# Performance work log

Measured on AMD Instinct MI355X. Metric: run time of the kernel, lower is better.

The kernel has to match this reference:

```python
import jax, jax.numpy as jnp
import numpy as np

TEMPERATURE = 0.05
BETA = 1.0
LAMBDA_THRESHOLD = 0.7
EPS = 1e-8


def setup_inputs() -> dict:
    key = jax.random.key(0)
    k1, k2 = jax.random.split(key)
    B, D = 8192, 256
    features = jax.random.normal(k1, (B, D), dtype=jnp.float32)
    labels = jax.random.randint(k2, (B,), 0, 100, dtype=jnp.int64)
    return {"features": features, "labels": labels}


def reference(features, labels):
    B = features.shape[0]
    # L2-normalize rows
    f = features / jnp.linalg.norm(features, axis=1, keepdims=True)
    sim = jnp.matmul(f, f.T) / TEMPERATURE                      # [B, B]
    pos_mask = (labels[:, None] == labels[None, :]).astype(f.dtype)
    eye = jnp.eye(B, dtype=f.dtype)
    pos_mask = pos_mask - eye                                    # positives, no diagonal
    exp_sim = jnp.exp(sim) * (1.0 - eye)                         # diag zeroed
    denom = jnp.sum(exp_sim, axis=1, keepdims=True)              # [B, 1]
    # SCL term: -sum over positive pairs of log(exp_sim[i,j] / (denom_i + eps))
    # log(exp_sim/(denom+eps)) = sim - log(denom+eps) for off-diagonal entries
    per_pair = jnp.log(denom + EPS) - sim                        # [B, B]
    num_pos = jnp.sum(pos_mask)
    scl_loss = jnp.sum(pos_mask * per_pair)
    scl_loss = jnp.where(num_pos > 0, scl_loss / num_pos, 0.0)
    # Relaxation term: rows with too-similar positives
    high_sim = ((sim * TEMPERATURE) > LAMBDA_THRESHOLD) & (pos_mask > 0)
    high_f = high_sim.astype(f.dtype)
    row_sum = jnp.sum(exp_sim * high_f, axis=1)                  # [B]
    self_term = jnp.exp(jnp.asarray(1.0 / TEMPERATURE, dtype=f.dtype))
    row_log = jnp.where(row_sum > 0, jnp.log(row_sum + self_term), 0.0)
    n_high = jnp.sum(high_f)
    relax_loss = jnp.where(n_high > 0, jnp.sum(row_log) / n_high, 0.0)
    total = scl_loss + BETA * relax_loss
    return total
```

## Files before the change

### kernel.cpp

```cpp
#include <hip/hip_runtime.h>
#include <hip/hip_bf16.h>
#include <math.h>

typedef short bf16x8 __attribute__((ext_vector_type(8)));
typedef float f32x16 __attribute__((ext_vector_type(16)));

#define NB 8192
#define ND 256
#define NCLSR 100
#define BK 64
#define ES 136
#define INV_T 20.0f
#define LOG2E_T 28.853900817779268f
#define HI_THR 1.2026042e6f
#define SELF_TERM 4.85165195e8f


__global__ __launch_bounds__(256) void normalize_kernel(
    const float* __restrict__ feat, unsigned short* __restrict__ fb,
    float* __restrict__ hsum, float* __restrict__ nhighf,
    float* __restrict__ scal) {
    const int wave = threadIdx.x >> 6;
    const int lane = threadIdx.x & 63;
    const int row  = blockIdx.x * 4 + wave;
    float4 v = reinterpret_cast<const float4*>(feat + (size_t)row * ND)[lane];
    float ss = v.x * v.x + v.y * v.y + v.z * v.z + v.w * v.w;
    #pragma unroll
    for (int off = 32; off > 0; off >>= 1) ss += __shfl_xor(ss, off);
    const float inv = rsqrtf(ss);
    ushort4 o;
    __hip_bfloat16 h0 = __float2bfloat16(v.x * inv); o.x = *reinterpret_cast<unsigned short*>(&h0);
    __hip_bfloat16 h1 = __float2bfloat16(v.y * inv); o.y = *reinterpret_cast<unsigned short*>(&h1);
    __hip_bfloat16 h2 = __float2bfloat16(v.z * inv); o.z = *reinterpret_cast<unsigned short*>(&h2);
    __hip_bfloat16 h3 = __float2bfloat16(v.w * inv); o.w = *reinterpret_cast<unsigned short*>(&h3);
    reinterpret_cast<ushort4*>(fb + (size_t)row * ND)[lane] = o;
    if (blockIdx.x < 32) {
        const int i = (blockIdx.x << 8) + threadIdx.x;
        hsum[i] = 0.f;
        nhighf[i] = 0.f;
    } else if (blockIdx.x == 32 && threadIdx.x < 6) {
        scal[threadIdx.x] = 0.f;
    }
}

__global__ __launch_bounds__(512, 2) void sim_kernel(
    const unsigned short* __restrict__ fb, const int* __restrict__ labels,
    float* __restrict__ Q, float* __restrict__ hsum,
    float* __restrict__ nhighf, float* __restrict__ scal) {
    __shared__ __align__(16) unsigned short ldsU[128 * ES];
    __shared__ float ldsCol[2][128];
    __shared__ float ldsRowF[128];
    __shared__ int   ldsLab[256];
    __shared__ float ldsP[8];
    unsigned short* ldsA = ldsU;
    unsigned short* ldsB = ldsU + 128 * BK;
    unsigned short* ldsE = ldsU;

    const int t = blockIdx.x;
    int bi = (int)((sqrtf((float)(8 * t + 1)) - 1.0f) * 0.5f);
    while ((bi + 1) * (bi + 2) / 2 <= t) ++bi;
    while (bi * (bi + 1) / 2 > t) --bi;
    const int bj = t - bi * (bi + 1) / 2;
    const int I0 = bi << 7;
    const int J0 = bj << 7;
    const bool isdiag = (bi == bj);

    const int tid  = threadIdx.x;
    const int wave = tid >> 6;
    const int lane = tid & 63;
    const int wy = wave >> 2;
    const int wx = wave & 3;
    const int l31  = lane & 31;
    const int half = lane >> 5;

    if (tid < 128) ldsLab[tid] = labels[I0 + tid];
    else if (tid < 256) ldsLab[tid] = labels[J0 + tid - 128];

    int offRC[2];
    #pragma unroll
    for (int c = 0; c < 2; ++c) {
        const int Lg = (c << 6) + lane;
        const int row_loc = (wave << 4) + (Lg >> 3);
        const int g = (Lg & 7) ^ ((Lg >> 3) & 7);
        offRC[c] = row_loc * ND + (g << 3);
    }
    const unsigned short* baseA = fb + (size_t)I0 * ND;
    const unsigned short* baseB = fb + (size_t)J0 * ND;

    f32x16 acc[2];
    #pragma unroll
    for (int fy = 0; fy < 2; ++fy)
        #pragma unroll
        for (int e = 0; e < 16; ++e) acc[fy][e] = 0.f;

    for (int kk = 0; kk < ND; kk += BK) {
        __syncthreads();
        #pragma unroll
        for (int c = 0; c < 2; ++c) {
            __builtin_amdgcn_global_load_lds(
                (const __attribute__((address_space(1))) void*)(baseA + offRC[c] + kk),
                (__attribute__((address_space(3))) void*)(ldsA + (wave << 10) + (c << 9)),
                16, 0, 0);
            __builtin_amdgcn_global_load_lds(
                (const __attribute__((address_space(1))) void*)(baseB + offRC[c] + kk),
                (__attribute__((address_space(3))) void*)(ldsB + (wave << 10) + (c << 9)),
                16, 0, 0);
        }
        __syncthreads();

        #pragma unroll
        for (int s = 0; s < 4; ++s) {
            const int gp = ((s << 1) + half) ^ (l31 & 7);
            const int rowB = (wx << 5) + l31;
            bf16x8 b = *reinterpret_cast<const bf16x8*>(ldsB + rowB * BK + (gp << 3));
            bf16x8 a[2];
            #pragma unroll
            for (int fy = 0; fy < 2; ++fy) {
                const int rowA = (wy << 6) + (fy << 5) + l31;
                a[fy] = *reinterpret_cast<const bf16x8*>(ldsA + rowA * BK + (gp << 3));
            }
            #pragma unroll
            for (int fy = 0; fy < 2; ++fy)
                acc[fy] = __builtin_amdgcn_mfma_f32_32x32x16_bf16(a[fy], b, acc[fy], 0, 0, 0);
        }
    }
    __syncthreads();

    const int ccol = (wx << 5) + l31;
    const int lcol = ldsLab[128 + ccol];
    unsigned short* ePtr = ldsE + (half << 2) * ES + ccol;

    float cs = 0.f;
    float pp = 0.f;

    if (!isdiag) {
        #pragma unroll
        for (int fy = 0; fy < 2; ++fy) {
            const int rbase = (wy << 6) + (fy << 5) + (half << 2);
            int4 lr[4];
            #pragma unroll
            for (int g = 0; g < 4; ++g)
                lr[g] = *reinterpret_cast<const int4*>(&ldsLab[rbase + (g << 3)]);
            #pragma unroll
            for (int reg = 0; reg < 16; ++reg) {
                const int g = reg >> 2, idx = reg & 3;
                const int lrow = (idx == 0) ? lr[g].x : (idx == 1) ? lr[g].y
                               : (idx == 2) ? lr[g].z : lr[g].w;
                const float a = acc[fy][reg];
                const float e = exp2f(a * LOG2E_T);
                cs += e;
                if (lcol == lrow) pp += a;
                __hip_bfloat16 h = __float2bfloat16(e);
                const int roff = (wy << 6) + (fy << 5) + idx + (g << 3);
                ePtr[roff * ES] = *reinterpret_cast<unsigned short*>(&h);
            }
        }
    } else {
        #pragma unroll
        for (int fy = 0; fy < 2; ++fy) {
            const bool dband = (((wy << 1) + fy) == wx);
            #pragma unroll
            for (int reg = 0; reg < 16; ++reg) {
                const int rloc = (reg & 3) + ((reg >> 2) << 3) + (half << 2);
                const int row_local = (wy << 6) + (fy << 5) + rloc;
                const int lrow = ldsLab[row_local];
                const float a = acc[fy][reg];
                const bool diag_el = dband && (l31 == rloc);
                float e = exp2f(a * LOG2E_T);
                if (diag_el) e = 0.f;
                cs += e;
                if (lcol == lrow && !diag_el) pp += a;
                __hip_bfloat16 h = __float2bfloat16(e);
                ldsE[row_local * ES + ccol] = *reinterpret_cast<unsigned short*>(&h);
            }
        }
    }
    const int anyhigh = (cs > HI_THR);
    cs += __shfl_xor(cs, 32);
    if (half == 0) ldsCol[wy][ccol] = cs;
    #pragma unroll
    for (int off = 32; off > 0; off >>= 1) pp += __shfl_xor(pp, off);
    if (lane == 0) ldsP[wave] = pp;

    __syncthreads();

    if (wave < 4) {
        bf16x8 ones;
        #pragma unroll
        for (int j = 0; j < 8; ++j) ones[j] = (short)0x3F80;
        f32x16 rs;
        #pragma unroll
        for (int e = 0; e < 16; ++e) rs[e] = 0.f;
        const int rE = (wave << 5) + l31;
        const unsigned short* rPtr = ldsE + rE * ES + (half << 3);
        #pragma unroll
        for (int kc = 0; kc < 8; ++kc) {
            bf16x8 bE = *reinterpret_cast<const bf16x8*>(rPtr + (kc << 4));
            rs = __builtin_amdgcn_mfma_f32_32x32x16_bf16(ones, bE, rs, 0, 0, 0);
        }
        if (half == 0) ldsRowF[rE] = rs[0];
    }
    __syncthreads();

    if (tid < 128) {
        Q[(size_t)(bi * 64 + bj) * 128 + tid] = ldsRowF[tid];
    } else if (tid < 256 && !isdiag) {
        const int c2 = tid - 128;
        Q[(size_t)(bj * 64 + bi) * 128 + c2] = ldsCol[0][c2] + ldsCol[1][c2];
    }
    if (tid == 0) {
        const float scale = isdiag ? 1.f : 2.f;
        atomicAdd(&scal[0], (ldsP[0] + ldsP[1] + ldsP[2] + ldsP[3] +
                             ldsP[4] + ldsP[5] + ldsP[6] + ldsP[7]) * scale);
    }

    if (__any(anyhigh)) {
        #pragma unroll
        for (int fy = 0; fy < 2; ++fy) {
            const bool dband = isdiag && (((wy << 1) + fy) == wx);
            #pragma unroll
            for (int reg = 0; reg < 16; ++reg) {
                const int rloc = (reg & 3) + ((reg >> 2) << 3) + (half << 2);
                const int row_local = (wy << 6) + (fy << 5) + rloc;
                const int lrow = ldsLab[row_local];
                const float a = acc[fy][reg];
                const bool diag_el = dband && (l31 == rloc);
                if (a > 0.7f && lcol == lrow && !diag_el) {
                    const float e2 = exp2f(a * LOG2E_T);
                    atomicAdd(&hsum[I0 + row_local], e2);
                    atomicAdd(&nhighf[I0 + row_local], 1.f);
                    if (!isdiag) {
                        atomicAdd(&hsum[J0 + ccol], e2);
                        atomicAdd(&nhighf[J0 + ccol], 1.f);
                    }
                }
            }
        }
    }
}

__global__ __launch_bounds__(256) void finalize_kernel(
    const float* __restrict__ Q, const float* __restrict__ hsum,
    const float* __restrict__ nhighf, const int* __restrict__ labels,
    float* __restrict__ scal, float* __restrict__ out) {
    const int g = blockIdx.x;
    const int tid = threadIdx.x;
    __shared__ int cnt[128];
    if (tid < 128) cnt[tid] = 0;
    __syncthreads();
    for (int i = tid; i < NB; i += 256)
        atomicAdd(&cnt[labels[i]], 1);
    const int r = tid & 127;
    const int sh = tid >> 7;
    const float* base = Q + (size_t)g * 64 * 128;
    float s = 0.f;
    #pragma unroll 8
    for (int i = 0; i < 32; ++i)
        s += base[(size_t)(sh * 32 + i) * 128 + r];
    __shared__ float red[256];
    red[tid] = s;
    __syncthreads();
    float SL = 0.f, RL = 0.f, NH = 0.f, NT = 0.f;
    if (tid < 128) {
        const float denom = red[tid] + red[tid + 128];
        const int i = (g << 7) + tid;
        const float np = (float)(cnt[labels[i]] - 1);
        SL = np * logf(denom + 1e-8f);
        const float h = hsum[i];
        if (h > 0.f) RL = logf(h + SELF_TERM);
        NH = nhighf[i];
    }
    if (g == 0 && tid < NCLSR) {
        const float nc = (float)cnt[tid];
        NT = nc * (nc - 1.f);
    }
    #pragma unroll
    for (int off = 32; off > 0; off >>= 1) {
        SL += __shfl_xor(SL, off); RL += __shfl_xor(RL, off);
        NH += __shfl_xor(NH, off); NT += __shfl_xor(NT, off);
    }
    __shared__ float part[4][4];
    if ((tid & 63) == 0) {
        int w = tid >> 6;
        part[w][0] = SL; part[w][1] = RL; part[w][2] = NH; part[w][3] = NT;
    }
    __syncthreads();
    if (tid == 0) {
        float sl = part[0][0] + part[1][0] + part[2][0] + part[3][0];
        float rl = part[0][1] + part[1][1] + part[2][1] + part[3][1];
        float nh = part[0][2] + part[1][2] + part[2][2] + part[3][2];
        float nt = part[0][3] + part[1][3] + part[2][3] + part[3][3];
        atomicAdd(&scal[1], sl);
        atomicAdd(&scal[2], rl);
        atomicAdd(&scal[3], nh);
        if (g == 0) atomicAdd(&scal[4], nt);
        __threadfence();
        const int ticket = atomicAdd((int*)(scal + 5), 1);
        if (ticket == 63) {
            const float SLt = atomicAdd(&scal[1], 0.f);
            const float RLt = atomicAdd(&scal[2], 0.f);
            const float NHt = atomicAdd(&scal[3], 0.f);
            const float NTt = atomicAdd(&scal[4], 0.f);
            const float pos = atomicAdd(&scal[0], 0.f) * INV_T;
            const float scl   = (NTt > 0.f) ? (SLt - pos) / NTt : 0.f;
            const float relax = (NHt > 0.f) ? RLt / NHt : 0.f;
            out[0] = scl + relax;
        }
    }
}

extern "C" void kernel_launch(void* const* d_in, const int* in_sizes, int n_in,
                              void* d_out, int out_size, void* d_ws, size_t ws_size,
                              hipStream_t stream) {
    const float* feat  = (const float*)d_in[0];
    const int* labels  = (const int*)d_in[1];
    float* out = (float*)d_out;

    char* ws = (char*)d_ws;
    unsigned short* fb = (unsigned short*)ws;
    float* Q      = (float*)(ws + (size_t)NB * ND * sizeof(unsigned short));
    float* hsum   = Q + 64 * 64 * 128;
    float* nhighf = hsum + NB;
    float* scal   = nhighf + NB;

    normalize_kernel<<<NB / 4, 256, 0, stream>>>(feat, fb, hsum, nhighf, scal);
    sim_kernel<<<2080, 512, 0, stream>>>(fb, labels, Q, hsum, nhighf, scal);
    finalize_kernel<<<64, 256, 0, stream>>>(Q, hsum, nhighf, labels, scal, out);
}
```

Baseline: 119.0 us.

## Fuse normalize, similarity and finalize into one cooperative persistent kernel

Merges the three kernels into one cooperatively launched persistent kernel. Grid-wide syncs separate the normalization phase, the tile loop and the final reduction. Blocks loop over the 2080 triangular tiles with a grid sized from occupancy (blocks per CU times 256), and the finalize phase runs on the first 64 blocks with 512 threads. This removes two kernel launches and their gaps, at the cost of grid-sync overhead, a persistent tile loop that may balance work less evenly, and cooperative-launch occupancy limits.

```diff
diff --git a/kernel.cpp b/kernel.cpp
--- a/kernel.cpp
+++ b/kernel.cpp
@@ -1,6 +1,9 @@
 #include <hip/hip_runtime.h>
 #include <hip/hip_bf16.h>
+#include <hip/hip_cooperative_groups.h>
 #include <math.h>
+
+namespace cg = cooperative_groups;
 
 typedef short bf16x8 __attribute__((ext_vector_type(8)));
 typedef float f32x16 __attribute__((ext_vector_type(16)));
@@ -10,43 +13,18 @@
 #define NCLSR 100
 #define BK 64
 #define ES 136
+#define NTILE 2080
 #define INV_T 20.0f
 #define LOG2E_T 28.853900817779268f
 #define HI_THR 1.2026042e6f
 #define SELF_TERM 4.85165195e8f
 
 
-__global__ __launch_bounds__(256) void normalize_kernel(
-    const float* __restrict__ feat, unsigned short* __restrict__ fb,
+__global__ __launch_bounds__(512, 2) void fused_kernel(
+    const float* __restrict__ feat, const int* __restrict__ labels,
+    unsigned short* __restrict__ fb, float* __restrict__ Q,
     float* __restrict__ hsum, float* __restrict__ nhighf,
-    float* __restrict__ scal) {
-    const int wave = threadIdx.x >> 6;
-    const int lane = threadIdx.x & 63;
-    const int row  = blockIdx.x * 4 + wave;
-    float4 v = reinterpret_cast<const float4*>(feat + (size_t)row * ND)[lane];
-    float ss = v.x * v.x + v.y * v.y + v.z * v.z + v.w * v.w;
-    #pragma unroll
-    for (int off = 32; off > 0; off >>= 1) ss += __shfl_xor(ss, off);
-    const float inv = rsqrtf(ss);
-    ushort4 o;
-    __hip_bfloat16 h0 = __float2bfloat16(v.x * inv); o.x = *reinterpret_cast<unsigned short*>(&h0);
-    __hip_bfloat16 h1 = __float2bfloat16(v.y * inv); o.y = *reinterpret_cast<unsigned short*>(&h1);
-    __hip_bfloat16 h2 = __float2bfloat16(v.z * inv); o.z = *reinterpret_cast<unsigned short*>(&h2);
-    __hip_bfloat16 h3 = __float2bfloat16(v.w * inv); o.w = *reinterpret_cast<unsigned short*>(&h3);
-    reinterpret_cast<ushort4*>(fb + (size_t)row * ND)[lane] = o;
-    if (blockIdx.x < 32) {
-        const int i = (blockIdx.x << 8) + threadIdx.x;
-        hsum[i] = 0.f;
-        nhighf[i] = 0.f;
-    } else if (blockIdx.x == 32 && threadIdx.x < 6) {
-        scal[threadIdx.x] = 0.f;
-    }
-}
-
-__global__ __launch_bounds__(512, 2) void sim_kernel(
-    const unsigned short* __restrict__ fb, const int* __restrict__ labels,
-    float* __restrict__ Q, float* __restrict__ hsum,
-    float* __restrict__ nhighf, float* __restrict__ scal) {
+    float* __restrict__ scal, float* __restrict__ out) {
     __shared__ __align__(16) unsigned short ldsU[128 * ES];
     __shared__ float ldsCol[2][128];
     __shared__ float ldsRowF[128];
@@ -56,15 +34,6 @@
     unsigned short* ldsB = ldsU + 128 * BK;
     unsigned short* ldsE = ldsU;
 
-    const int t = blockIdx.x;
-    int bi = (int)((sqrtf((float)(8 * t + 1)) - 1.0f) * 0.5f);
-    while ((bi + 1) * (bi + 2) / 2 <= t) ++bi;
-    while (bi * (bi + 1) / 2 > t) --bi;
-    const int bj = t - bi * (bi + 1) / 2;
-    const int I0 = bi << 7;
-    const int J0 = bj << 7;
-    const bool isdiag = (bi == bj);
-
     const int tid  = threadIdx.x;
     const int wave = tid >> 6;
     const int lane = tid & 63;
@@ -73,8 +42,26 @@
     const int l31  = lane & 31;
     const int half = lane >> 5;
 
-    if (tid < 128) ldsLab[tid] = labels[I0 + tid];
-    else if (tid < 256) ldsLab[tid] = labels[J0 + tid - 128];
+    for (int row = blockIdx.x * 8 + wave; row < NB; row += gridDim.x * 8) {
+        float4 v = reinterpret_cast<const float4*>(feat + (size_t)row * ND)[lane];
+        float ss = v.x * v.x + v.y * v.y + v.z * v.z + v.w * v.w;
+        #pragma unroll
+        for (int off = 32; off > 0; off >>= 1) ss += __shfl_xor(ss, off);
+        const float inv = rsqrtf(ss);
+        ushort4 o;
+        __hip_bfloat16 h0 = __float2bfloat16(v.x * inv); o.x = *reinterpret_cast<unsigned short*>(&h0);
+        __hip_bfloat16 h1 = __float2bfloat16(v.y * inv); o.y = *reinterpret_cast<unsigned short*>(&h1);
+        __hip_bfloat16 h2 = __float2bfloat16(v.z * inv); o.z = *reinterpret_cast<unsigned short*>(&h2);
+        __hip_bfloat16 h3 = __float2bfloat16(v.w * inv); o.w = *reinterpret_cast<unsigned short*>(&h3);
+        reinterpret_cast<ushort4*>(fb + (size_t)row * ND)[lane] = o;
+    }
+    for (int i = blockIdx.x * 512 + tid; i < NB; i += gridDim.x * 512) {
+        hsum[i] = 0.f;
+        nhighf[i] = 0.f;
+    }
+    if (blockIdx.x == 0 && tid < 6) scal[tid] = 0.f;
+    __threadfence();
+    cg::this_grid().sync();
 
     int offRC[2];
     #pragma unroll
@@ -84,227 +71,242 @@
         const int g = (Lg & 7) ^ ((Lg >> 3) & 7);
         offRC[c] = row_loc * ND + (g << 3);
     }
-    const unsigned short* baseA = fb + (size_t)I0 * ND;
-    const unsigned short* baseB = fb + (size_t)J0 * ND;
-
-    f32x16 acc[2];
-    #pragma unroll
-    for (int fy = 0; fy < 2; ++fy)
+
+    for (int t = blockIdx.x; t < NTILE; t += gridDim.x) {
+        __syncthreads();
+
+        int bi = (int)((sqrtf((float)(8 * t + 1)) - 1.0f) * 0.5f);
+        while ((bi + 1) * (bi + 2) / 2 <= t) ++bi;
+        while (bi * (bi + 1) / 2 > t) --bi;
+        const int bj = t - bi * (bi + 1) / 2;
+        const int I0 = bi << 7;
+        const int J0 = bj << 7;
+        const bool isdiag = (bi == bj);
+
+        if (tid < 128) ldsLab[tid] = labels[I0 + tid];
+        else if (tid < 256) ldsLab[tid] = labels[J0 + tid - 128];
+
+        const unsigned short* baseA = fb + (size_t)I0 * ND;
+        const unsigned short* baseB = fb + (size_t)J0 * ND;
+
+        f32x16 acc[2];
         #pragma unroll
-        for (int e = 0; e < 16; ++e) acc[fy][e] = 0.f;
-
-    for (int kk = 0; kk < ND; kk += BK) {
-        __syncthreads();
+        for (int fy = 0; fy < 2; ++fy)
+            #pragma unroll
+            for (int e = 0; e < 16; ++e) acc[fy][e] = 0.f;
+
+        for (int kk = 0; kk < ND; kk += BK) {
+            __syncthreads();
+            #pragma unroll
+            for (int c = 0; c < 2; ++c) {
+                __builtin_amdgcn_global_load_lds(
+                    (const __attribute__((address_space(1))) void*)(baseA + offRC[c] + kk),
+                    (__attribute__((address_space(3))) void*)(ldsA + (wave << 10) + (c << 9)),
+                    16, 0, 0);
+                __builtin_amdgcn_global_load_lds(
+                    (const __attribute__((address_space(1))) void*)(baseB + offRC[c] + kk),
+                    (__attribute__((address_space(3))) void*)(ldsB + (wave << 10) + (c << 9)),
+                    16, 0, 0);
+            }
+            __syncthreads();
+
+            #pragma unroll
+            for (int s = 0; s < 4; ++s) {
+                const int gp = ((s << 1) + half) ^ (l31 & 7);
+                const int rowB = (wx << 5) + l31;
+                bf16x8 b = *reinterpret_cast<const bf16x8*>(ldsB + rowB * BK + (gp << 3));
+                bf16x8 a[2];
+                #pragma unroll
+                for (int fy = 0; fy < 2; ++fy) {
+                    const int rowA = (wy << 6) + (fy << 5) + l31;
+                    a[fy] = *reinterpret_cast<const bf16x8*>(ldsA + rowA * BK + (gp << 3));
+                }
+                #pragma unroll
+                for (int fy = 0; fy < 2; ++fy)
+                    acc[fy] = __builtin_amdgcn_mfma_f32_32x32x16_bf16(a[fy], b, acc[fy], 0, 0, 0);
+            }
+        }
+        __syncthreads();
+
+        const int ccol = (wx << 5) + l31;
+        const int lcol = ldsLab[128 + ccol];
+        unsigned short* ePtr = ldsE + (half << 2) * ES + ccol;
+
+        float cs = 0.f;
+        float pp = 0.f;
+
+        if (!isdiag) {
+            #pragma unroll
+            for (int fy = 0; fy < 2; ++fy) {
+                const int rbase = (wy << 6) + (fy << 5) + (half << 2);
+                int4 lr[4];
+                #pragma unroll
+                for (int g = 0; g < 4; ++g)
+                    lr[g] = *reinterpret_cast<const int4*>(&ldsLab[rbase + (g << 3)]);
+                #pragma unroll
+                for (int reg = 0; reg < 16; ++reg) {
+                    const int g = reg >> 2, idx = reg & 3;
+                    const int lrow = (idx == 0) ? lr[g].x : (idx == 1) ? lr[g].y
+                                   : (idx == 2) ? lr[g].z : lr[g].w;
+                    const float a = acc[fy][reg];
+                    const float e = exp2f(a * LOG2E_T);
+                    cs += e;
+                    if (lcol == lrow) pp += a;
+                    __hip_bfloat16 h = __float2bfloat16(e);
+                    const int roff = (wy << 6) + (fy << 5) + idx + (g << 3);
+                    ePtr[roff * ES] = *reinterpret_cast<unsigned short*>(&h);
+                }
+            }
+        } else {
+            #pragma unroll
+            for (int fy = 0; fy < 2; ++fy) {
+                const bool dband = (((wy << 1) + fy) == wx);
+                #pragma unroll
+                for (int reg = 0; reg < 16; ++reg) {
+                    const int rloc = (reg & 3) + ((reg >> 2) << 3) + (half << 2);
+                    const int row_local = (wy << 6) + (fy << 5) + rloc;
+                    const int lrow = ldsLab[row_local];
+                    const float a = acc[fy][reg];
+                    const bool diag_el = dband && (l31 == rloc);
+                    float e = exp2f(a * LOG2E_T);
+                    if (diag_el) e = 0.f;
+                    cs += e;
+                    if (lcol == lrow && !diag_el) pp += a;
+                    __hip_bfloat16 h = __float2bfloat16(e);
+                    ldsE[row_local * ES + ccol] = *reinterpret_cast<unsigned short*>(&h);
+                }
+            }
+        }
+        const int anyhigh = (cs > HI_THR);
+        cs += __shfl_xor(cs, 32);
+        if (half == 0) ldsCol[wy][ccol] = cs;
         #pragma unroll
-        for (int c = 0; c < 2; ++c) {
-            __builtin_amdgcn_global_load_lds(
-                (const __attribute__((address_space(1))) void*)(baseA + offRC[c] + kk),
-                (__attribute__((address_space(3))) void*)(ldsA + (wave << 10) + (c << 9)),
-                16, 0, 0);
-            __builtin_amdgcn_global_load_lds(
-                (const __attribute__((address_space(1))) void*)(baseB + offRC[c] + kk),
-                (__attribute__((address_space(3))) void*)(ldsB + (wave << 10) + (c << 9)),
-                16, 0, 0);
-        }
-        __syncthreads();
-
-        #pragma unroll
-        for (int s = 0; s < 4; ++s) {
-            const int gp = ((s << 1) + half) ^ (l31 & 7);
-            const int rowB = (wx << 5) + l31;
-            bf16x8 b = *reinterpret_cast<const bf16x8*>(ldsB + rowB * BK + (gp << 3));
-            bf16x8 a[2];
+        for (int off = 32; off > 0; off >>= 1) pp += __shfl_xor(pp, off);
+        if (lane == 0) ldsP[wave] = pp;
+
+        if (__any(anyhigh)) {
             #pragma unroll
             for (int fy = 0; fy < 2; ++fy) {
-                const int rowA = (wy << 6) + (fy << 5) + l31;
-                a[fy] = *reinterpret_cast<const bf16x8*>(ldsA + rowA * BK + (gp << 3));
-            }
-            #pragma unroll
-            for (int fy = 0; fy < 2; ++fy)
-                acc[fy] = __builtin_amdgcn_mfma_f32_32x32x16_bf16(a[fy], b, acc[fy], 0, 0, 0);
-        }
-    }
-    __syncthreads();
-
-    const int ccol = (wx << 5) + l31;
-    const int lcol = ldsLab[128 + ccol];
-    unsigned short* ePtr = ldsE + (half << 2) * ES + ccol;
-
-    float cs = 0.f;
-    float pp = 0.f;
-
-    if (!isdiag) {
-        #pragma unroll
-        for (int fy = 0; fy < 2; ++fy) {
-            const int rbase = (wy << 6) + (fy << 5) + (half << 2);
-            int4 lr[4];
-            #pragma unroll
-            for (int g = 0; g < 4; ++g)
-                lr[g] = *reinterpret_cast<const int4*>(&ldsLab[rbase + (g << 3)]);
-            #pragma unroll
-            for (int reg = 0; reg < 16; ++reg) {
-                const int g = reg >> 2, idx = reg & 3;
-                const int lrow = (idx == 0) ? lr[g].x : (idx == 1) ? lr[g].y
-                               : (idx == 2) ? lr[g].z : lr[g].w;
-                const float a = acc[fy][reg];
-                const float e = exp2f(a * LOG2E_T);
-                cs += e;
-                if (lcol == lrow) pp += a;
-                __hip_bfloat16 h = __float2bfloat16(e);
-                const int roff = (wy << 6) + (fy << 5) + idx + (g << 3);
-                ePtr[roff * ES] = *reinterpret_cast<unsigned short*>(&h);
-            }
-        }
-    } else {
-        #pragma unroll
-        for (int fy = 0; fy < 2; ++fy) {
-            const bool dband = (((wy << 1) + fy) == wx);
-            #pragma unroll
-            for (int reg = 0; reg < 16; ++reg) {
-                const int rloc = (reg & 3) + ((reg >> 2) << 3) + (half << 2);
-                const int row_local = (wy << 6) + (fy << 5) + rloc;
-                const int lrow = ldsLab[row_local];
-                const float a = acc[fy][reg];
-                const bool diag_el = dband && (l31 == rloc);
-                float e = exp2f(a * LOG2E_T);
-                if (diag_el) e = 0.f;
-                cs += e;
-                if (lcol == lrow && !diag_el) pp += a;
-                __hip_bfloat16 h = __float2bfloat16(e);
-                ldsE[row_local * ES + ccol] = *reinterpret_cast<unsigned short*>(&h);
-            }
-        }
-    }
-    const int anyhigh = (cs > HI_THR);
-    cs += __shfl_xor(cs, 32);
-    if (half == 0) ldsCol[wy][ccol] = cs;
-    #pragma unroll
-    for (int off = 32; off > 0; off >>= 1) pp += __shfl_xor(pp, off);
-    if (lane == 0) ldsP[wave] = pp;
-
-    __syncthreads();
-
-    if (wave < 4) {
-        bf16x8 ones;
-        #pragma unroll
-        for (int j = 0; j < 8; ++j) ones[j] = (short)0x3F80;
-        f32x16 rs;
-        #pragma unroll
-        for (int e = 0; e < 16; ++e) rs[e] = 0.f;
-        const int rE = (wave << 5) + l31;
-        const unsigned short* rPtr = ldsE + rE * ES + (half << 3);
-        #pragma unroll
-        for (int kc = 0; kc < 8; ++kc) {
-            bf16x8 bE = *reinterpret_cast<const bf16x8*>(rPtr + (kc << 4));
-            rs = __builtin_amdgcn_mfma_f32_32x32x16_bf16(ones, bE, rs, 0, 0, 0);
-        }
-        if (half == 0) ldsRowF[rE] = rs[0];
-    }
-    __syncthreads();
-
-    if (tid < 128) {
-        Q[(size_t)(bi * 64 + bj) * 128 + tid] = ldsRowF[tid];
-    } else if (tid < 256 && !isdiag) {
-        const int c2 = tid - 128;
-        Q[(size_t)(bj * 64 + bi) * 128 + c2] = ldsCol[0][c2] + ldsCol[1][c2];
-    }
-    if (tid == 0) {
-        const float scale = isdiag ? 1.f : 2.f;
-        atomicAdd(&scal[0], (ldsP[0] + ldsP[1] + ldsP[2] + ldsP[3] +
-                             ldsP[4] + ldsP[5] + ldsP[6] + ldsP[7]) * scale);
-    }
-
-    if (__any(anyhigh)) {
-        #pragma unroll
-        for (int fy = 0; fy < 2; ++fy) {
-            const bool dband = isdiag && (((wy << 1) + fy) == wx);
-            #pragma unroll
-            for (int reg = 0; reg < 16; ++reg) {
-                const int rloc = (reg & 3) + ((reg >> 2) << 3) + (half << 2);
-                const int row_local = (wy << 6) + (fy << 5) + rloc;
-                const int lrow = ldsLab[row_local];
-                const float a = acc[fy][reg];
-                const bool diag_el = dband && (l31 == rloc);
-                if (a > 0.7f && lcol == lrow && !diag_el) {
-                    const float e2 = exp2f(a * LOG2E_T);
-                    atomicAdd(&hsum[I0 + row_local], e2);
-                    atomicAdd(&nhighf[I0 + row_local], 1.f);
-                    if (!isdiag) {
-                        atomicAdd(&hsum[J0 + ccol], e2);
-                        atomicAdd(&nhighf[J0 + ccol], 1.f);
+                const bool dband = isdiag && (((wy << 1) + fy) == wx);
+                #pragma unroll
+                for (int reg = 0; reg < 16; ++reg) {
+                    const int rloc = (reg & 3) + ((reg >> 2) << 3) + (half << 2);
+                    const int row_local = (wy << 6) + (fy << 5) + rloc;
+                    const int lrow = ldsLab[row_local];
+                    const float a = acc[fy][reg];
+                    const bool diag_el = dband && (l31 == rloc);
+                    if (a > 0.7f && lcol == lrow && !diag_el) {
+                        const float e2 = exp2f(a * LOG2E_T);
+                        atomicAdd(&hsum[I0 + row_local], e2);
+                        atomicAdd(&nhighf[I0 + row_local], 1.f);
+                        if (!isdiag) {
+                            atomicAdd(&hsum[J0 + ccol], e2);
+                            atomicAdd(&nhighf[J0 + ccol], 1.f);
+                        }
                     }
                 }
             }
         }
-    }
-}
-
-__global__ __launch_bounds__(256) void finalize_kernel(
-    const float* __restrict__ Q, const float* __restrict__ hsum,
-    const float* __restrict__ nhighf, const int* __restrict__ labels,
-    float* __restrict__ scal, float* __restrict__ out) {
-    const int g = blockIdx.x;
-    const int tid = threadIdx.x;
-    __shared__ int cnt[128];
-    if (tid < 128) cnt[tid] = 0;
-    __syncthreads();
-    for (int i = tid; i < NB; i += 256)
-        atomicAdd(&cnt[labels[i]], 1);
-    const int r = tid & 127;
-    const int sh = tid >> 7;
-    const float* base = Q + (size_t)g * 64 * 128;
-    float s = 0.f;
-    #pragma unroll 8
-    for (int i = 0; i < 32; ++i)
-        s += base[(size_t)(sh * 32 + i) * 128 + r];
-    __shared__ float red[256];
-    red[tid] = s;
-    __syncthreads();
-    float SL = 0.f, RL = 0.f, NH = 0.f, NT = 0.f;
-    if (tid < 128) {
-        const float denom = red[tid] + red[tid + 128];
-        const int i = (g << 7) + tid;
-        const float np = (float)(cnt[labels[i]] - 1);
-        SL = np * logf(denom + 1e-8f);
-        const float h = hsum[i];
-        if (h > 0.f) RL = logf(h + SELF_TERM);
-        NH = nhighf[i];
-    }
-    if (g == 0 && tid < NCLSR) {
-        const float nc = (float)cnt[tid];
-        NT = nc * (nc - 1.f);
-    }
-    #pragma unroll
-    for (int off = 32; off > 0; off >>= 1) {
-        SL += __shfl_xor(SL, off); RL += __shfl_xor(RL, off);
-        NH += __shfl_xor(NH, off); NT += __shfl_xor(NT, off);
-    }
-    __shared__ float part[4][4];
-    if ((tid & 63) == 0) {
-        int w = tid >> 6;
-        part[w][0] = SL; part[w][1] = RL; part[w][2] = NH; part[w][3] = NT;
-    }
-    __syncthreads();
-    if (tid == 0) {
-        float sl = part[0][0] + part[1][0] + part[2][0] + part[3][0];
-        float rl = part[0][1] + part[1][1] + part[2][1] + part[3][1];
-        float nh = part[0][2] + part[1][2] + part[2][2] + part[3][2];
-        float nt = part[0][3] + part[1][3] + part[2][3] + part[3][3];
-        atomicAdd(&scal[1], sl);
-        atomicAdd(&scal[2], rl);
-        atomicAdd(&scal[3], nh);
-        if (g == 0) atomicAdd(&scal[4], nt);
-        __threadfence();
-        const int ticket = atomicAdd((int*)(scal + 5), 1);
-        if (ticket == 63) {
-            const float SLt = atomicAdd(&scal[1], 0.f);
-            const float RLt = atomicAdd(&scal[2], 0.f);
-            const float NHt = atomicAdd(&scal[3], 0.f);
-            const float NTt = atomicAdd(&scal[4], 0.f);
-            const float pos = atomicAdd(&scal[0], 0.f) * INV_T;
-            const float scl   = (NTt > 0.f) ? (SLt - pos) / NTt : 0.f;
-            const float relax = (NHt > 0.f) ? RLt / NHt : 0.f;
-            out[0] = scl + relax;
+        __syncthreads();
+
+        if (wave < 4) {
+            bf16x8 ones;
+            #pragma unroll
+            for (int j = 0; j < 8; ++j) ones[j] = (short)0x3F80;
+            f32x16 rs;
+            #pragma unroll
+            for (int e = 0; e < 16; ++e) rs[e] = 0.f;
+            const int rE = (wave << 5) + l31;
+            const unsigned short* rPtr = ldsE + rE * ES + (half << 3);
+            #pragma unroll
+            for (int kc = 0; kc < 8; ++kc) {
+                bf16x8 bE = *reinterpret_cast<const bf16x8*>(rPtr + (kc << 4));
+                rs = __builtin_amdgcn_mfma_f32_32x32x16_bf16(ones, bE, rs, 0, 0, 0);
+            }
+            if (half == 0) ldsRowF[rE] = rs[0];
+        }
+        __syncthreads();
+
+        if (tid < 128) {
+            Q[(size_t)(bi * 64 + bj) * 128 + tid] = ldsRowF[tid];
+        } else if (tid < 256 && !isdiag) {
+            const int c2 = tid - 128;
+            Q[(size_t)(bj * 64 + bi) * 128 + c2] = ldsCol[0][c2] + ldsCol[1][c2];
+        }
+        if (tid == 0) {
+            const float scale = isdiag ? 1.f : 2.f;
+            atomicAdd(&scal[0], (ldsP[0] + ldsP[1] + ldsP[2] + ldsP[3] +
+                                 ldsP[4] + ldsP[5] + ldsP[6] + ldsP[7]) * scale);
+        }
+    }
+    __threadfence();
+    cg::this_grid().sync();
+
+    if (blockIdx.x < 64) {
+        const int g = blockIdx.x;
+        int*   cnt  = (int*)ldsU;
+        float* red  = (float*)ldsU + 128;
+        float* part = (float*)ldsU + 640;
+        if (tid < 128) cnt[tid] = 0;
+        __syncthreads();
+        for (int i = tid; i < NB; i += 512)
+            atomicAdd(&cnt[labels[i]], 1);
+        const int r  = tid & 127;
+        const int sh = tid >> 7;
+        const float* base = Q + (size_t)g * 64 * 128;
+        float s = 0.f;
+        #pragma unroll 4
+        for (int i = 0; i < 16; ++i)
+            s += base[(size_t)(sh * 16 + i) * 128 + r];
+        red[tid] = s;
+        __syncthreads();
+        float SL = 0.f, RL = 0.f, NH = 0.f, NT = 0.f;
+        if (tid < 128) {
+            const float denom = red[tid] + red[tid + 128] + red[tid + 256] + red[tid + 384];
+            const int i = (g << 7) + tid;
+            const float np = (float)(cnt[labels[i]] - 1);
+            SL = np * logf(denom + 1e-8f);
+            const float h = hsum[i];
+            if (h > 0.f) RL = logf(h + SELF_TERM);
+            NH = nhighf[i];
+        }
+        if (g == 0 && tid < NCLSR) {
+            const float nc = (float)cnt[tid];
+            NT = nc * (nc - 1.f);
+        }
+        #pragma unroll
+        for (int off = 32; off > 0; off >>= 1) {
+            SL += __shfl_xor(SL, off); RL += __shfl_xor(RL, off);
+            NH += __shfl_xor(NH, off); NT += __shfl_xor(NT, off);
+        }
+        if (lane == 0) {
+            part[wave * 4 + 0] = SL; part[wave * 4 + 1] = RL;
+            part[wave * 4 + 2] = NH; part[wave * 4 + 3] = NT;
+        }
+        __syncthreads();
+        if (tid == 0) {
+            float sl = 0.f, rl = 0.f, nh = 0.f, nt = 0.f;
+            #pragma unroll
+            for (int w = 0; w < 8; ++w) {
+                sl += part[w * 4 + 0]; rl += part[w * 4 + 1];
+                nh += part[w * 4 + 2]; nt += part[w * 4 + 3];
+            }
+            atomicAdd(&scal[1], sl);
+            atomicAdd(&scal[2], rl);
+            atomicAdd(&scal[3], nh);
+            if (g == 0) atomicAdd(&scal[4], nt);
+            __threadfence();
+            const int ticket = atomicAdd((int*)(scal + 5), 1);
+            if (ticket == 63) {
+                const float SLt = atomicAdd(&scal[1], 0.f);
+                const float RLt = atomicAdd(&scal[2], 0.f);
+                const float NHt = atomicAdd(&scal[3], 0.f);
+                const float NTt = atomicAdd(&scal[4], 0.f);
+                const float pos = atomicAdd(&scal[0], 0.f) * INV_T;
+                const float scl   = (NTt > 0.f) ? (SLt - pos) / NTt : 0.f;
+                const float relax = (NHt > 0.f) ? RLt / NHt : 0.f;
+                out[0] = scl + relax;
+            }
         }
     }
 }
@@ -323,7 +325,13 @@
     float* nhighf = hsum + NB;
     float* scal   = nhighf + NB;
 
-    normalize_kernel<<<NB / 4, 256, 0, stream>>>(feat, fb, hsum, nhighf, scal);
-    sim_kernel<<<2080, 512, 0, stream>>>(fb, labels, Q, hsum, nhighf, scal);
-    finalize_kernel<<<64, 256, 0, stream>>>(Q, hsum, nhighf, labels, scal, out);
+    int nb = 0;
+    hipOccupancyMaxActiveBlocksPerMultiprocessor(&nb, fused_kernel, 512, 0);
+    if (nb < 1) nb = 1;
+    int grid = nb * 256;
+    if (grid > NTILE) grid = NTILE;
+
+    void* args[] = {(void*)&feat, (void*)&labels, (void*)&fb, (void*)&Q,
+                    (void*)&hsum, (void*)&nhighf, (void*)&scal, (void*)&out};
+    hipLaunchCooperativeKernel(fused_kernel, dim3(grid), dim3(512), args, 0, stream);
 }
```

Measured after the change: 278.4 us. 134% more time.

## Use 4 waves per block with 64x64 wave tiles in sim kernel

Applied to the files above, without the earlier changes.

Shrinks the sim kernel block from 8 waves to 4 waves. Each wave now computes a 2x2 grid of 32x32 MFMA tiles, so every A and B fragment read from LDS is reused across two MFMAs. The high-similarity atomic pass also moves ahead of the row-sum barrier. This cuts LDS read traffic per MFMA and removes a barrier-idle phase, at the cost of more accumulator registers per wave and fewer waves available to hide latency.

```diff
diff --git a/kernel.cpp b/kernel.cpp
--- a/kernel.cpp
+++ b/kernel.cpp
@@ -43,7 +43,7 @@
     }
 }
 
-__global__ __launch_bounds__(512, 2) void sim_kernel(
+__global__ __launch_bounds__(256, 2) void sim_kernel(
     const unsigned short* __restrict__ fb, const int* __restrict__ labels,
     float* __restrict__ Q, float* __restrict__ hsum,
     float* __restrict__ nhighf, float* __restrict__ scal) {
@@ -51,7 +51,7 @@
     __shared__ float ldsCol[2][128];
     __shared__ float ldsRowF[128];
     __shared__ int   ldsLab[256];
-    __shared__ float ldsP[8];
+    __shared__ float ldsP[4];
     unsigned short* ldsA = ldsU;
     unsigned short* ldsB = ldsU + 128 * BK;
     unsigned short* ldsE = ldsU;
@@ -68,42 +68,44 @@
     const int tid  = threadIdx.x;
     const int wave = tid >> 6;
     const int lane = tid & 63;
-    const int wy = wave >> 2;
-    const int wx = wave & 3;
+    const int wy = wave >> 1;
+    const int wx = wave & 1;
     const int l31  = lane & 31;
     const int half = lane >> 5;
 
     if (tid < 128) ldsLab[tid] = labels[I0 + tid];
-    else if (tid < 256) ldsLab[tid] = labels[J0 + tid - 128];
-
-    int offRC[2];
-    #pragma unroll
-    for (int c = 0; c < 2; ++c) {
+    else           ldsLab[tid] = labels[J0 + tid - 128];
+
+    int offRC[4];
+    #pragma unroll
+    for (int c = 0; c < 4; ++c) {
         const int Lg = (c << 6) + lane;
-        const int row_loc = (wave << 4) + (Lg >> 3);
+        const int row_loc = (wave << 5) + (Lg >> 3);
         const int g = (Lg & 7) ^ ((Lg >> 3) & 7);
         offRC[c] = row_loc * ND + (g << 3);
     }
     const unsigned short* baseA = fb + (size_t)I0 * ND;
     const unsigned short* baseB = fb + (size_t)J0 * ND;
 
-    f32x16 acc[2];
+    f32x16 acc[2][2];
     #pragma unroll
     for (int fy = 0; fy < 2; ++fy)
         #pragma unroll
-        for (int e = 0; e < 16; ++e) acc[fy][e] = 0.f;
+        for (int fx = 0; fx < 2; ++fx)
+            #pragma unroll
+            for (int e = 0; e < 16; ++e) acc[fy][fx][e] = 0.f;
 
     for (int kk = 0; kk < ND; kk += BK) {
         __syncthreads();
         #pragma unroll
-        for (int c = 0; c < 2; ++c) {
+        for (int c = 0; c < 4; ++c) {
             __builtin_amdgcn_global_load_lds(
                 (const __attribute__((address_space(1))) void*)(baseA + offRC[c] + kk),
-                (__attribute__((address_space(3))) void*)(ldsA + (wave << 10) + (c << 9)),
+                (__attribute__((address_space(3))) void*)(ldsA + (wave << 11) + (c << 9)),
                 16, 0, 0);
             __builtin_amdgcn_global_load_lds(
                 (const __attribute__((address_space(1))) void*)(baseB + offRC[c] + kk),
-                (__attribute__((address_space(3))) void*)(ldsB + (wave << 10) + (c << 9)),
+                (__attribute__((address_space(3))) void*)(ldsB + (wave << 11) + (c << 9)),
                 16, 0, 0);
         }
         __syncthreads();
@@ -111,26 +113,34 @@
         #pragma unroll
         for (int s = 0; s < 4; ++s) {
             const int gp = ((s << 1) + half) ^ (l31 & 7);
-            const int rowB = (wx << 5) + l31;
-            bf16x8 b = *reinterpret_cast<const bf16x8*>(ldsB + rowB * BK + (gp << 3));
-            bf16x8 a[2];
-            #pragma unroll
-            for (int fy = 0; fy < 2; ++fy) {
-                const int rowA = (wy << 6) + (fy << 5) + l31;
-                a[fy] = *reinterpret_cast<const bf16x8*>(ldsA + rowA * BK + (gp << 3));
+            bf16x8 a[2], b[2];
+            #pragma unroll
+            for (int f = 0; f < 2; ++f) {
+                const int rowA = (wy << 6) + (f << 5) + l31;
+                const int rowB = (wx << 6) + (f << 5) + l31;
+                a[f] = *reinterpret_cast<const bf16x8*>(ldsA + rowA * BK + (gp << 3));
+                b[f] = *reinterpret_cast<const bf16x8*>(ldsB + rowB * BK + (gp << 3));
             }
             #pragma unroll
             for (int fy = 0; fy < 2; ++fy)
-                acc[fy] = __builtin_amdgcn_mfma_f32_32x32x16_bf16(a[fy], b, acc[fy], 0, 0, 0);
-        }
-    }
-    __syncthreads();
-
-    const int ccol = (wx << 5) + l31;
-    const int lcol = ldsLab[128 + ccol];
-    unsigned short* ePtr = ldsE + (half << 2) * ES + ccol;
-
-    float cs = 0.f;
+                #pragma unroll
+                for (int fx = 0; fx < 2; ++fx)
+                    acc[fy][fx] = __builtin_amdgcn_mfma_f32_32x32x16_bf16(
+                        a[fy], b[fx], acc[fy][fx], 0, 0, 0);
+        }
+    }
+    __syncthreads();
+
+    int ccol[2], lcol[2];
+    #pragma unroll
+    for (int fx = 0; fx < 2; ++fx) {
+        ccol[fx] = (wx << 6) + (fx << 5) + l31;
+        lcol[fx] = ldsLab[128 + ccol[fx]];
+    }
+    unsigned short* ePtr0 = ldsE + (half << 2) * ES + ccol[0];
+    unsigned short* ePtr1 = ldsE + (half << 2) * ES + ccol[1];
+
+    float cs[2] = {0.f, 0.f};
     float pp = 0.f;
 
     if (!isdiag) {
@@ -146,96 +156,107 @@
                 const int g = reg >> 2, idx = reg & 3;
                 const int lrow = (idx == 0) ? lr[g].x : (idx == 1) ? lr[g].y
                                : (idx == 2) ? lr[g].z : lr[g].w;
-                const float a = acc[fy][reg];
-                const float e = exp2f(a * LOG2E_T);
-                cs += e;
-                if (lcol == lrow) pp += a;
-                __hip_bfloat16 h = __float2bfloat16(e);
                 const int roff = (wy << 6) + (fy << 5) + idx + (g << 3);
-                ePtr[roff * ES] = *reinterpret_cast<unsigned short*>(&h);
+                #pragma unroll
+                for (int fx = 0; fx < 2; ++fx) {
+                    const float a = acc[fy][fx][reg];
+                    const float e = exp2f(a * LOG2E_T);
+                    cs[fx] += e;
+                    if (lcol[fx] == lrow) pp += a;
+                    __hip_bfloat16 h = __float2bfloat16(e);
+                    (fx ? ePtr1 : ePtr0)[roff * ES] = *reinterpret_cast<unsigned short*>(&h);
+                }
             }
         }
     } else {
         #pragma unroll
         for (int fy = 0; fy < 2; ++fy) {
-            const bool dband = (((wy << 1) + fy) == wx);
             #pragma unroll
             for (int reg = 0; reg < 16; ++reg) {
                 const int rloc = (reg & 3) + ((reg >> 2) << 3) + (half << 2);
                 const int row_local = (wy << 6) + (fy << 5) + rloc;
                 const int lrow = ldsLab[row_local];
-                const float a = acc[fy][reg];
-                const bool diag_el = dband && (l31 == rloc);
-                float e = exp2f(a * LOG2E_T);
-                if (diag_el) e = 0.f;
-                cs += e;
-                if (lcol == lrow && !diag_el) pp += a;
-                __hip_bfloat16 h = __float2bfloat16(e);
-                ldsE[row_local * ES + ccol] = *reinterpret_cast<unsigned short*>(&h);
+                #pragma unroll
+                for (int fx = 0; fx < 2; ++fx) {
+                    const bool dband = (((wy << 1) + fy) == ((wx << 1) + fx));
+                    const bool diag_el = dband && (l31 == rloc);
+                    const float a = acc[fy][fx][reg];
+                    float e = exp2f(a * LOG2E_T);
+                    if (diag_el) e = 0.f;
+                    cs[fx] += e;
+                    if (lcol[fx] == lrow && !diag_el) pp += a;
+                    __hip_bfloat16 h = __float2bfloat16(e);
+                    ldsE[row_local * ES + ccol[fx]] = *reinterpret_cast<unsigned short*>(&h);
+                }
             }
         }
     }
-    const int anyhigh = (cs > HI_THR);
-    cs += __shfl_xor(cs, 32);
-    if (half == 0) ldsCol[wy][ccol] = cs;
+    const int anyhigh = (cs[0] > HI_THR) || (cs[1] > HI_THR);
+    #pragma unroll
+    for (int fx = 0; fx < 2; ++fx) cs[fx] += __shfl_xor(cs[fx], 32);
+    if (half == 0) {
+        ldsCol[wy][ccol[0]] = cs[0];
+        ldsCol[wy][ccol[1]] = cs[1];
+    }
     #pragma unroll
     for (int off = 32; off > 0; off >>= 1) pp += __shfl_xor(pp, off);
     if (lane == 0) ldsP[wave] = pp;
 
-    __syncthreads();
-
-    if (wave < 4) {
-        bf16x8 ones;
-        #pragma unroll
-        for (int j = 0; j < 8; ++j) ones[j] = (short)0x3F80;
-        f32x16 rs;
-        #pragma unroll
-        for (int e = 0; e < 16; ++e) rs[e] = 0.f;
-        const int rE = (wave << 5) + l31;
-        const unsigned short* rPtr = ldsE + rE * ES + (half << 3);
-        #pragma unroll
-        for (int kc = 0; kc < 8; ++kc) {
-            bf16x8 bE = *reinterpret_cast<const bf16x8*>(rPtr + (kc << 4));
-            rs = __builtin_amdgcn_mfma_f32_32x32x16_bf16(ones, bE, rs, 0, 0, 0);
-        }
-        if (half == 0) ldsRowF[rE] = rs[0];
-    }
-    __syncthreads();
-
-    if (tid < 128) {
-        Q[(size_t)(bi * 64 + bj) * 128 + tid] = ldsRowF[tid];
-    } else if (tid < 256 && !isdiag) {
-        const int c2 = tid - 128;
-        Q[(size_t)(bj * 64 + bi) * 128 + c2] = ldsCol[0][c2] + ldsCol[1][c2];
-    }
-    if (tid == 0) {
-        const float scale = isdiag ? 1.f : 2.f;
-        atomicAdd(&scal[0], (ldsP[0] + ldsP[1] + ldsP[2] + ldsP[3] +
-                             ldsP[4] + ldsP[5] + ldsP[6] + ldsP[7]) * scale);
-    }
-
     if (__any(anyhigh)) {
         #pragma unroll
         for (int fy = 0; fy < 2; ++fy) {
-            const bool dband = isdiag && (((wy << 1) + fy) == wx);
             #pragma unroll
             for (int reg = 0; reg < 16; ++reg) {
                 const int rloc = (reg & 3) + ((reg >> 2) << 3) + (half << 2);
                 const int row_local = (wy << 6) + (fy << 5) + rloc;
                 const int lrow = ldsLab[row_local];
-                const float a = acc[fy][reg];
-                const bool diag_el = dband && (l31 == rloc);
-                if (a > 0.7f && lcol == lrow && !diag_el) {
-                    const float e2 = exp2f(a * LOG2E_T);
-                    atomicAdd(&hsum[I0 + row_local], e2);
-                    atomicAdd(&nhighf[I0 + row_local], 1.f);
-                    if (!isdiag) {
-                        atomicAdd(&hsum[J0 + ccol], e2);
-                        atomicAdd(&nhighf[J0 + ccol], 1.f);
+                #pragma unroll
+                for (int fx = 0; fx < 2; ++fx) {
+                    const bool dband = isdiag && (((wy << 1) + fy) == ((wx << 1) + fx));
+                    const bool diag_el = dband && (l31 == rloc);
+                    const float a = acc[fy][fx][reg];
+                    if (a > 0.7f && lcol[fx] == lrow && !diag_el) {
+                        const float e2 = exp2f(a * LOG2E_T);
+                        atomicAdd(&hsum[I0 + row_local], e2);
+                        atomicAdd(&nhighf[I0 + row_local], 1.f);
+                        if (!isdiag) {
+                            atomicAdd(&hsum[J0 + ccol[fx]], e2);
+                            atomicAdd(&nhighf[J0 + ccol[fx]], 1.f);
+                        }
                     }
                 }
             }
         }
+    }
+    __syncthreads();
+
+    {
+        bf16x8 ones;
+        #pragma unroll
+        for (int j = 0; j < 8; ++j) ones[j] = (short)0x3F80;
+        f32x16 rs;
+        #pragma unroll
+        for (int e = 0; e < 16; ++e) rs[e] = 0.f;
+        const int rE = (wave << 5) + l31;
+        const unsigned short* rPtr = ldsE + rE * ES + (half << 3);
+        #pragma unroll
+        for (int kc = 0; kc < 8; ++kc) {
+            bf16x8 bE = *reinterpret_cast<const bf16x8*>(rPtr + (kc << 4));
+            rs = __builtin_amdgcn_mfma_f32_32x32x16_bf16(ones, bE, rs, 0, 0, 0);
+        }
+        if (half == 0) ldsRowF[rE] = rs[0];
+    }
+    __syncthreads();
+
+    if (tid < 128) {
+        Q[(size_t)(bi * 64 + bj) * 128 + tid] = ldsRowF[tid];
+    } else if (!isdiag) {
+        const int c2 = tid - 128;
+        Q[(size_t)(bj * 64 + bi) * 128 + c2] = ldsCol[0][c2] + ldsCol[1][c2];
+    }
+    if (tid == 0) {
+        const float scale = isdiag ? 1.f : 2.f;
+        atomicAdd(&scal[0], (ldsP[0] + ldsP[1] + ldsP[2] + ldsP[3]) * scale);
     }
 }
 
@@ -324,6 +345,6 @@
     float* scal   = nhighf + NB;
 
     normalize_kernel<<<NB / 4, 256, 0, stream>>>(feat, fb, hsum, nhighf, scal);
-    sim_kernel<<<2080, 512, 0, stream>>>(fb, labels, Q, hsum, nhighf, scal);
+    sim_kernel<<<2080, 256, 0, stream>>>(fb, labels, Q, hsum, nhighf, scal);
     finalize_kernel<<<64, 256, 0, stream>>>(Q, hsum, nhighf, labels, scal, out);
 }
```

Result: no change. 117.1 us (median of 2 runs) (-1.6%).
